# Kernel optimization log

Hardware: AMD Instinct MI355X
Metric: run time of the kernel (lower is better)

Reference implementation:

```python
import jax, jax.numpy as jnp
import numpy as np

N_STATIONS = 276
CONTEXT_LEN = 384  # args.context_len * 2
TARGET_LEN = 96
BATCH = 4096


def setup_inputs() -> dict:
    key = jax.random.key(0)
    k1, k2, k3, k4, k5, k6 = jax.random.split(key, 6)
    z = jax.random.normal(k1, (BATCH, CONTEXT_LEN), dtype=jnp.float32)
    stations = jax.random.randint(k2, (BATCH,), 0, N_STATIONS, dtype=jnp.int64)
    # per-station Linear params (nn.Linear(context_len, target_len) x n_stations)
    lim = 1.0 / np.sqrt(CONTEXT_LEN)
    W = jax.random.uniform(k3, (N_STATIONS, TARGET_LEN, CONTEXT_LEN), jnp.float32, -lim, lim)
    b = jax.random.uniform(k4, (N_STATIONS, TARGET_LEN), jnp.float32, -lim, lim)
    loc = jax.random.normal(k5, (N_STATIONS,), dtype=jnp.float32)
    scale = jax.random.uniform(k6, (N_STATIONS,), jnp.float32, 0.5, 2.0)
    return {"z": z, "stations": stations, "W": W, "b": b, "loc": loc, "scale": scale}


def reference(z, stations, W, b, loc, scale):
    # norm: (z - loc[i]) / scale[i]
    loc_i = loc[stations][:, None]      # (bs, 1)
    scale_i = scale[stations][:, None]  # (bs, 1)
    zn = (z - loc_i) / scale_i          # (bs, context_len)
    # per-sample station-specific Linear: batched GEMV via gathered weights
    out = jnp.einsum("boi,bi->bo", W[stations], zn) + b[stations]  # (bs, target_len)
    # denorm then softplus
    out = out * scale_i + loc_i
    return jax.nn.softplus(out)
```

## Files before the change

### kernel.cpp

```cpp
#include <hip/hip_runtime.h>
#include <math.h>

#define N_STATIONS 276
#define CTX 384
#define TGT 96
#define BATCH 4096
#define NTILE_N 6
#define NBLK (N_STATIONS * NTILE_N)

typedef __attribute__((ext_vector_type(8))) short bf16x8;
typedef __attribute__((ext_vector_type(4))) float f32x4;

__device__ __forceinline__ short f2bf(float f) {
    unsigned u = __builtin_bit_cast(unsigned, f);
    u = (u + 0x7FFFu + ((u >> 16) & 1u)) >> 16;
    return (short)u;
}
__device__ __forceinline__ float bf2f(short h) {
    unsigned u = ((unsigned)(unsigned short)h) << 16;
    return __builtin_bit_cast(float, u);
}

__global__ __launch_bounds__(1024) void build_lists(
    const int* __restrict__ stations,
    int* __restrict__ order,
    int* __restrict__ offsets)
{
    __shared__ int cnt[N_STATIONS];
    __shared__ int cnt2[N_STATIONS];
    __shared__ int poff[N_STATIONS + 1];
    const int tid = threadIdx.x;
    for (int i = tid; i < N_STATIONS; i += 1024) { cnt[i] = 0; cnt2[i] = 0; }
    __syncthreads();
    for (int b = tid; b < BATCH; b += 1024) atomicAdd(&cnt[stations[b]], 1);
    __syncthreads();
    if (tid < 64) {
        int run = 0;
        for (int base = 0; base < N_STATIONS; base += 64) {
            const int i = base + tid;
            int v = (i < N_STATIONS) ? cnt[i] : 0;
#pragma unroll
            for (int off = 1; off < 64; off <<= 1) {
                int u = __shfl_up(v, off, 64);
                if (tid >= off) v += u;
            }
            if (i < N_STATIONS) poff[i + 1] = run + v;
            run += __shfl(v, 63, 64);
        }
        if (tid == 0) poff[0] = 0;
    }
    __syncthreads();
    for (int b = tid; b < BATCH; b += 1024) {
        int s = stations[b];
        int p = atomicAdd(&cnt2[s], 1);
        order[poff[s] + p] = b;
    }
    if (tid <= N_STATIONS) offsets[tid] = poff[tid];
}

__device__ __forceinline__ void cvt_hilo(float4 a, float4 b, bf16x8& hi, bf16x8& lo) {
    float f[8] = {a.x, a.y, a.z, a.w, b.x, b.y, b.z, b.w};
#pragma unroll
    for (int i = 0; i < 8; ++i) {
        short h = f2bf(f[i]);
        hi[i] = h;
        lo[i] = f2bf(f[i] - bf2f(h));
    }
}
__device__ __forceinline__ bf16x8 cvt_norm(float4 a, float4 b, float lc, float inv) {
    float f[8] = {a.x, a.y, a.z, a.w, b.x, b.y, b.z, b.w};
    bf16x8 r;
#pragma unroll
    for (int i = 0; i < 8; ++i) r[i] = f2bf((f[i] - lc) * inv);
    return r;
}

__global__ __launch_bounds__(64) void nlinear_mfma(
    const float* __restrict__ z,
    const int*   __restrict__ order,
    const int*   __restrict__ offsets,
    const float* __restrict__ W,
    const float* __restrict__ bias,
    const float* __restrict__ loc,
    const float* __restrict__ scale,
    float*       __restrict__ out)
{
    const int bid = blockIdx.x;
    const int s   = bid / NTILE_N;
    const int nt  = bid - s * NTILE_N;
    const int n0  = nt * 16;

    const int start = offsets[s];
    const int m     = offsets[s + 1] - start;
    if (m == 0) return;

    const int l  = threadIdx.x;
    const int lr = l & 15;
    const int kh = (l >> 4) * 8;

    const float lc = loc[s], sc = scale[s], inv = 1.0f / sc;

    const float* wrow  = W + ((size_t)s * TGT + n0 + lr) * CTX + kh;
    const float  biasv = bias[(size_t)s * TGT + n0 + lr];

    const int ntiles = (m + 15) >> 4;
    const int rbase  = (l >> 4) * 4;

    for (int t0 = 0; t0 < ntiles; t0 += 2) {
        int j0 = t0 * 16 + lr;        if (j0 > m - 1) j0 = m - 1;
        int j1 = t0 * 16 + 16 + lr;   if (j1 > m - 1) j1 = m - 1;
        const float* zr0 = z + (size_t)order[start + j0] * CTX + kh;
        const float* zr1 = z + (size_t)order[start + j1] * CTX + kh;
        const bool two = (t0 + 1 < ntiles);

        f32x4 acc0 = {0.f, 0.f, 0.f, 0.f};
        f32x4 acc1 = {0.f, 0.f, 0.f, 0.f};

#pragma unroll
        for (int kk = 0; kk < 12; ++kk) {
            const int ko = kk * 32;
            float4 wv0 = *reinterpret_cast<const float4*>(wrow + ko);
            float4 wv1 = *reinterpret_cast<const float4*>(wrow + ko + 4);
            float4 a00 = *reinterpret_cast<const float4*>(zr0 + ko);
            float4 a01 = *reinterpret_cast<const float4*>(zr0 + ko + 4);

            bf16x8 bhi, blo;
            cvt_hilo(wv0, wv1, bhi, blo);
            bf16x8 afr0 = cvt_norm(a00, a01, lc, inv);

            acc0 = __builtin_amdgcn_mfma_f32_16x16x32_bf16(afr0, bhi, acc0, 0, 0, 0);
            acc0 = __builtin_amdgcn_mfma_f32_16x16x32_bf16(afr0, blo, acc0, 0, 0, 0);

            if (two) {
                float4 a10 = *reinterpret_cast<const float4*>(zr1 + ko);
                float4 a11 = *reinterpret_cast<const float4*>(zr1 + ko + 4);
                bf16x8 afr1 = cvt_norm(a10, a11, lc, inv);
                acc1 = __builtin_amdgcn_mfma_f32_16x16x32_bf16(afr1, bhi, acc1, 0, 0, 0);
                acc1 = __builtin_amdgcn_mfma_f32_16x16x32_bf16(afr1, blo, acc1, 0, 0, 0);
            }
        }

#pragma unroll
        for (int r = 0; r < 4; ++r) {
            int j = t0 * 16 + rbase + r;
            if (j < m) {
                int id = order[start + j];
                float v = (acc0[r] + biasv) * sc + lc;
                out[(size_t)id * TGT + n0 + lr] =
                    fmaxf(v, 0.f) + log1pf(expf(-fabsf(v)));
            }
        }
        if (two) {
#pragma unroll
            for (int r = 0; r < 4; ++r) {
                int j = t0 * 16 + 16 + rbase + r;
                if (j < m) {
                    int id = order[start + j];
                    float v = (acc1[r] + biasv) * sc + lc;
                    out[(size_t)id * TGT + n0 + lr] =
                        fmaxf(v, 0.f) + log1pf(expf(-fabsf(v)));
                }
            }
        }
    }
}

extern "C" void kernel_launch(void* const* d_in, const int* in_sizes, int n_in,
                              void* d_out, int out_size, void* d_ws, size_t ws_size,
                              hipStream_t stream) {
    const float* z        = (const float*)d_in[0];
    const int*   stations = (const int*)  d_in[1];
    const float* W        = (const float*)d_in[2];
    const float* bias     = (const float*)d_in[3];
    const float* loc      = (const float*)d_in[4];
    const float* scale    = (const float*)d_in[5];
    float* out = (float*)d_out;

    int* order   = (int*)d_ws;
    int* offsets = order + BATCH;

    build_lists<<<1, 1024, 0, stream>>>(stations, order, offsets);
    nlinear_mfma<<<NBLK, 64, 0, stream>>>(z, order, offsets, W, bias, loc, scale, out);
}
```

Baseline: 32.37 us.

## Fuse station list building into GEMV kernel via per-block ballot scan

Removes the separate single-block build_lists launch. Each block now scans all 4096 station ids with wave ballots and builds its own sample list in shared memory. This drops one kernel launch and the serialized one-block prologue, but every block re-reads the stations array, and the list is capped at 256 entries per station. The change also remaps block ids for XCD locality, uses fma-based normalization and the library bf16 conversion, and reduces inner-loop unrolling to 4.

```diff
diff --git a/kernel.cpp b/kernel.cpp
--- a/kernel.cpp
+++ b/kernel.cpp
@@ -1,4 +1,5 @@
 #include <hip/hip_runtime.h>
+#include <hip/hip_bf16.h>
 #include <math.h>
 
 #define N_STATIONS 276
@@ -7,55 +8,18 @@
 #define BATCH 4096
 #define NTILE_N 6
 #define NBLK (N_STATIONS * NTILE_N)
+#define CPX (NBLK / 8)
+#define LISTMAX 256
 
 typedef __attribute__((ext_vector_type(8))) short bf16x8;
 typedef __attribute__((ext_vector_type(4))) float f32x4;
 
 __device__ __forceinline__ short f2bf(float f) {
-    unsigned u = __builtin_bit_cast(unsigned, f);
-    u = (u + 0x7FFFu + ((u >> 16) & 1u)) >> 16;
-    return (short)u;
+    return (short)__builtin_bit_cast(unsigned short, __float2bfloat16(f));
 }
 __device__ __forceinline__ float bf2f(short h) {
     unsigned u = ((unsigned)(unsigned short)h) << 16;
     return __builtin_bit_cast(float, u);
-}
-
-__global__ __launch_bounds__(1024) void build_lists(
-    const int* __restrict__ stations,
-    int* __restrict__ order,
-    int* __restrict__ offsets)
-{
-    __shared__ int cnt[N_STATIONS];
-    __shared__ int cnt2[N_STATIONS];
-    __shared__ int poff[N_STATIONS + 1];
-    const int tid = threadIdx.x;
-    for (int i = tid; i < N_STATIONS; i += 1024) { cnt[i] = 0; cnt2[i] = 0; }
-    __syncthreads();
-    for (int b = tid; b < BATCH; b += 1024) atomicAdd(&cnt[stations[b]], 1);
-    __syncthreads();
-    if (tid < 64) {
-        int run = 0;
-        for (int base = 0; base < N_STATIONS; base += 64) {
-            const int i = base + tid;
-            int v = (i < N_STATIONS) ? cnt[i] : 0;
-#pragma unroll
-            for (int off = 1; off < 64; off <<= 1) {
-                int u = __shfl_up(v, off, 64);
-                if (tid >= off) v += u;
-            }
-            if (i < N_STATIONS) poff[i + 1] = run + v;
-            run += __shfl(v, 63, 64);
-        }
-        if (tid == 0) poff[0] = 0;
-    }
-    __syncthreads();
-    for (int b = tid; b < BATCH; b += 1024) {
-        int s = stations[b];
-        int p = atomicAdd(&cnt2[s], 1);
-        order[poff[s] + p] = b;
-    }
-    if (tid <= N_STATIONS) offsets[tid] = poff[tid];
 }
 
 __device__ __forceinline__ void cvt_hilo(float4 a, float4 b, bf16x8& hi, bf16x8& lo) {
@@ -67,38 +31,50 @@
         lo[i] = f2bf(f[i] - bf2f(h));
     }
 }
-__device__ __forceinline__ bf16x8 cvt_norm(float4 a, float4 b, float lc, float inv) {
+__device__ __forceinline__ bf16x8 cvt_norm(float4 a, float4 b, float inv, float nb) {
     float f[8] = {a.x, a.y, a.z, a.w, b.x, b.y, b.z, b.w};
     bf16x8 r;
 #pragma unroll
-    for (int i = 0; i < 8; ++i) r[i] = f2bf((f[i] - lc) * inv);
+    for (int i = 0; i < 8; ++i) r[i] = f2bf(fmaf(f[i], inv, nb));
     return r;
 }
 
-__global__ __launch_bounds__(64) void nlinear_mfma(
+__global__ __launch_bounds__(64) void nlinear_fused(
     const float* __restrict__ z,
-    const int*   __restrict__ order,
-    const int*   __restrict__ offsets,
+    const int*   __restrict__ stations,
     const float* __restrict__ W,
     const float* __restrict__ bias,
     const float* __restrict__ loc,
     const float* __restrict__ scale,
     float*       __restrict__ out)
 {
-    const int bid = blockIdx.x;
-    const int s   = bid / NTILE_N;
-    const int nt  = bid - s * NTILE_N;
-    const int n0  = nt * 16;
+    __shared__ int list[LISTMAX];
 
-    const int start = offsets[s];
-    const int m     = offsets[s + 1] - start;
-    if (m == 0) return;
+    const int bid0 = blockIdx.x;
+    const int bid  = (bid0 & 7) * CPX + (bid0 >> 3);
+    const int s    = bid / NTILE_N;
+    const int n0   = (bid - s * NTILE_N) * 16;
 
     const int l  = threadIdx.x;
     const int lr = l & 15;
     const int kh = (l >> 4) * 8;
 
+    int m = 0;
+    const unsigned long long lanelt = (1ull << l) - 1ull;
+    for (int c = 0; c < BATCH; c += 64) {
+        const bool match = (stations[c + l] == s);
+        const unsigned long long msk = __ballot(match);
+        if (match) {
+            const int pos = m + (int)__popcll(msk & lanelt);
+            if (pos < LISTMAX) list[pos] = c + l;
+        }
+        m += (int)__popcll(msk);
+    }
+    if (m == 0) return;
+    if (m > LISTMAX) m = LISTMAX;
+
     const float lc = loc[s], sc = scale[s], inv = 1.0f / sc;
+    const float nb = -lc * inv;
 
     const float* wrow  = W + ((size_t)s * TGT + n0 + lr) * CTX + kh;
     const float  biasv = bias[(size_t)s * TGT + n0 + lr];
@@ -109,14 +85,14 @@
     for (int t0 = 0; t0 < ntiles; t0 += 2) {
         int j0 = t0 * 16 + lr;        if (j0 > m - 1) j0 = m - 1;
         int j1 = t0 * 16 + 16 + lr;   if (j1 > m - 1) j1 = m - 1;
-        const float* zr0 = z + (size_t)order[start + j0] * CTX + kh;
-        const float* zr1 = z + (size_t)order[start + j1] * CTX + kh;
+        const float* zr0 = z + (size_t)list[j0] * CTX + kh;
+        const float* zr1 = z + (size_t)list[j1] * CTX + kh;
         const bool two = (t0 + 1 < ntiles);
 
         f32x4 acc0 = {0.f, 0.f, 0.f, 0.f};
         f32x4 acc1 = {0.f, 0.f, 0.f, 0.f};
 
-#pragma unroll
+#pragma unroll 4
         for (int kk = 0; kk < 12; ++kk) {
             const int ko = kk * 32;
             float4 wv0 = *reinterpret_cast<const float4*>(wrow + ko);
@@ -126,7 +102,7 @@
 
             bf16x8 bhi, blo;
             cvt_hilo(wv0, wv1, bhi, blo);
-            bf16x8 afr0 = cvt_norm(a00, a01, lc, inv);
+            bf16x8 afr0 = cvt_norm(a00, a01, inv, nb);
 
             acc0 = __builtin_amdgcn_mfma_f32_16x16x32_bf16(afr0, bhi, acc0, 0, 0, 0);
             acc0 = __builtin_amdgcn_mfma_f32_16x16x32_bf16(afr0, blo, acc0, 0, 0, 0);
@@ -134,7 +110,7 @@
             if (two) {
                 float4 a10 = *reinterpret_cast<const float4*>(zr1 + ko);
                 float4 a11 = *reinterpret_cast<const float4*>(zr1 + ko + 4);
-                bf16x8 afr1 = cvt_norm(a10, a11, lc, inv);
+                bf16x8 afr1 = cvt_norm(a10, a11, inv, nb);
                 acc1 = __builtin_amdgcn_mfma_f32_16x16x32_bf16(afr1, bhi, acc1, 0, 0, 0);
                 acc1 = __builtin_amdgcn_mfma_f32_16x16x32_bf16(afr1, blo, acc1, 0, 0, 0);
             }
@@ -142,9 +118,9 @@
 
 #pragma unroll
         for (int r = 0; r < 4; ++r) {
-            int j = t0 * 16 + rbase + r;
+            const int j = t0 * 16 + rbase + r;
             if (j < m) {
-                int id = order[start + j];
+                const int id = list[j];
                 float v = (acc0[r] + biasv) * sc + lc;
                 out[(size_t)id * TGT + n0 + lr] =
                     fmaxf(v, 0.f) + log1pf(expf(-fabsf(v)));
@@ -153,9 +129,9 @@
         if (two) {
 #pragma unroll
             for (int r = 0; r < 4; ++r) {
-                int j = t0 * 16 + 16 + rbase + r;
+                const int j = t0 * 16 + 16 + rbase + r;
                 if (j < m) {
-                    int id = order[start + j];
+                    const int id = list[j];
                     float v = (acc1[r] + biasv) * sc + lc;
                     out[(size_t)id * TGT + n0 + lr] =
                         fmaxf(v, 0.f) + log1pf(expf(-fabsf(v)));
@@ -176,9 +152,5 @@
     const float* scale    = (const float*)d_in[5];
     float* out = (float*)d_out;
 
-    int* order   = (int*)d_ws;
-    int* offsets = order + BATCH;
-
-    build_lists<<<1, 1024, 0, stream>>>(stations, order, offsets);
-    nlinear_mfma<<<NBLK, 64, 0, stream>>>(z, order, offsets, W, bias, loc, scale, out);
+    nlinear_fused<<<NBLK, 64, 0, stream>>>(z, stations, W, bias, loc, scale, out);
 }
```

Result: slower. 40.79 us (+26.0%).

## Split K across blocks with atomic accumulation and separate epilogue kernel

Applied to the files above, without the earlier changes.

The GEMV work is split in two along the context dimension, which doubles the block count. Each half hoists its weight hi/lo bf16 conversion into registers once per block, and blocks are remapped so they spread across XCDs. Partial sums are combined with atomicAdd into a zeroed output, and bias, denorm and softplus move to a new elementwise epilogue kernel. This raises parallelism for the small per-station GEMV, at the cost of a memset, an extra kernel launch, atomic traffic and a second pass over the output.

```diff
diff --git a/kernel.cpp b/kernel.cpp
--- a/kernel.cpp
+++ b/kernel.cpp
@@ -1,4 +1,5 @@
 #include <hip/hip_runtime.h>
+#include <hip/hip_bf16.h>
 #include <math.h>
 
 #define N_STATIONS 276
@@ -6,19 +7,37 @@
 #define TGT 96
 #define BATCH 4096
 #define NTILE_N 6
-#define NBLK (N_STATIONS * NTILE_N)
+#define KSPLIT 2
+#define KHALF 192
+#define NSTEP 6
+#define NTASK (N_STATIONS * NTILE_N * KSPLIT)
+#define CPX2 (NTASK / 8)
 
 typedef __attribute__((ext_vector_type(8))) short bf16x8;
 typedef __attribute__((ext_vector_type(4))) float f32x4;
 
 __device__ __forceinline__ short f2bf(float f) {
-    unsigned u = __builtin_bit_cast(unsigned, f);
-    u = (u + 0x7FFFu + ((u >> 16) & 1u)) >> 16;
-    return (short)u;
+    return (short)__builtin_bit_cast(unsigned short, __float2bfloat16(f));
 }
 __device__ __forceinline__ float bf2f(short h) {
     unsigned u = ((unsigned)(unsigned short)h) << 16;
     return __builtin_bit_cast(float, u);
+}
+__device__ __forceinline__ void cvt_hilo(float4 a, float4 b, bf16x8& hi, bf16x8& lo) {
+    float f[8] = {a.x, a.y, a.z, a.w, b.x, b.y, b.z, b.w};
+#pragma unroll
+    for (int i = 0; i < 8; ++i) {
+        short h = f2bf(f[i]);
+        hi[i] = h;
+        lo[i] = f2bf(f[i] - bf2f(h));
+    }
+}
+__device__ __forceinline__ bf16x8 cvt_norm(float4 a, float4 b, float inv, float nb) {
+    float f[8] = {a.x, a.y, a.z, a.w, b.x, b.y, b.z, b.w};
+    bf16x8 r;
+#pragma unroll
+    for (int i = 0; i < 8; ++i) r[i] = f2bf(fmaf(f[i], inv, nb));
+    return r;
 }
 
 __global__ __launch_bounds__(1024) void build_lists(
@@ -58,37 +77,21 @@
     if (tid <= N_STATIONS) offsets[tid] = poff[tid];
 }
 
-__device__ __forceinline__ void cvt_hilo(float4 a, float4 b, bf16x8& hi, bf16x8& lo) {
-    float f[8] = {a.x, a.y, a.z, a.w, b.x, b.y, b.z, b.w};
-#pragma unroll
-    for (int i = 0; i < 8; ++i) {
-        short h = f2bf(f[i]);
-        hi[i] = h;
-        lo[i] = f2bf(f[i] - bf2f(h));
-    }
-}
-__device__ __forceinline__ bf16x8 cvt_norm(float4 a, float4 b, float lc, float inv) {
-    float f[8] = {a.x, a.y, a.z, a.w, b.x, b.y, b.z, b.w};
-    bf16x8 r;
-#pragma unroll
-    for (int i = 0; i < 8; ++i) r[i] = f2bf((f[i] - lc) * inv);
-    return r;
-}
-
-__global__ __launch_bounds__(64) void nlinear_mfma(
+__global__ __launch_bounds__(64, 1) void nlinear_splitk(
     const float* __restrict__ z,
     const int*   __restrict__ order,
     const int*   __restrict__ offsets,
     const float* __restrict__ W,
-    const float* __restrict__ bias,
     const float* __restrict__ loc,
     const float* __restrict__ scale,
     float*       __restrict__ out)
 {
-    const int bid = blockIdx.x;
-    const int s   = bid / NTILE_N;
-    const int nt  = bid - s * NTILE_N;
-    const int n0  = nt * 16;
+    const int bid0 = blockIdx.x;
+    const int bid  = (bid0 & 7) * CPX2 + (bid0 >> 3);
+    const int half = bid & 1;
+    const int task = bid >> 1;
+    const int s    = task / NTILE_N;
+    const int n0   = (task - s * NTILE_N) * 16;
 
     const int start = offsets[s];
     const int m     = offsets[s + 1] - start;
@@ -98,71 +101,60 @@
     const int lr = l & 15;
     const int kh = (l >> 4) * 8;
 
-    const float lc = loc[s], sc = scale[s], inv = 1.0f / sc;
+    const float lc  = loc[s];
+    const float inv = 1.0f / scale[s];
+    const float nb  = -lc * inv;
 
-    const float* wrow  = W + ((size_t)s * TGT + n0 + lr) * CTX + kh;
-    const float  biasv = bias[(size_t)s * TGT + n0 + lr];
+    const float* wrow = W + ((size_t)s * TGT + n0 + lr) * CTX + half * KHALF + kh;
+    bf16x8 bhi[NSTEP], blo[NSTEP];
+#pragma unroll
+    for (int kk = 0; kk < NSTEP; ++kk) {
+        float4 w0 = *reinterpret_cast<const float4*>(wrow + kk * 32);
+        float4 w1 = *reinterpret_cast<const float4*>(wrow + kk * 32 + 4);
+        cvt_hilo(w0, w1, bhi[kk], blo[kk]);
+    }
 
     const int ntiles = (m + 15) >> 4;
     const int rbase  = (l >> 4) * 4;
 
-    for (int t0 = 0; t0 < ntiles; t0 += 2) {
-        int j0 = t0 * 16 + lr;        if (j0 > m - 1) j0 = m - 1;
-        int j1 = t0 * 16 + 16 + lr;   if (j1 > m - 1) j1 = m - 1;
-        const float* zr0 = z + (size_t)order[start + j0] * CTX + kh;
-        const float* zr1 = z + (size_t)order[start + j1] * CTX + kh;
-        const bool two = (t0 + 1 < ntiles);
+    for (int t = 0; t < ntiles; ++t) {
+        int j = t * 16 + lr; if (j > m - 1) j = m - 1;
+        const float* zr = z + (size_t)order[start + j] * CTX + half * KHALF + kh;
 
-        f32x4 acc0 = {0.f, 0.f, 0.f, 0.f};
-        f32x4 acc1 = {0.f, 0.f, 0.f, 0.f};
-
+        f32x4 acc = {0.f, 0.f, 0.f, 0.f};
 #pragma unroll
-        for (int kk = 0; kk < 12; ++kk) {
-            const int ko = kk * 32;
-            float4 wv0 = *reinterpret_cast<const float4*>(wrow + ko);
-            float4 wv1 = *reinterpret_cast<const float4*>(wrow + ko + 4);
-            float4 a00 = *reinterpret_cast<const float4*>(zr0 + ko);
-            float4 a01 = *reinterpret_cast<const float4*>(zr0 + ko + 4);
-
-            bf16x8 bhi, blo;
-            cvt_hilo(wv0, wv1, bhi, blo);
-            bf16x8 afr0 = cvt_norm(a00, a01, lc, inv);
-
-            acc0 = __builtin_amdgcn_mfma_f32_16x16x32_bf16(afr0, bhi, acc0, 0, 0, 0);
-            acc0 = __builtin_amdgcn_mfma_f32_16x16x32_bf16(afr0, blo, acc0, 0, 0, 0);
-
-            if (two) {
-                float4 a10 = *reinterpret_cast<const float4*>(zr1 + ko);
-                float4 a11 = *reinterpret_cast<const float4*>(zr1 + ko + 4);
-                bf16x8 afr1 = cvt_norm(a10, a11, lc, inv);
-                acc1 = __builtin_amdgcn_mfma_f32_16x16x32_bf16(afr1, bhi, acc1, 0, 0, 0);
-                acc1 = __builtin_amdgcn_mfma_f32_16x16x32_bf16(afr1, blo, acc1, 0, 0, 0);
-            }
+        for (int kk = 0; kk < NSTEP; ++kk) {
+            float4 a0 = *reinterpret_cast<const float4*>(zr + kk * 32);
+            float4 a1 = *reinterpret_cast<const float4*>(zr + kk * 32 + 4);
+            bf16x8 af = cvt_norm(a0, a1, inv, nb);
+            acc = __builtin_amdgcn_mfma_f32_16x16x32_bf16(af, bhi[kk], acc, 0, 0, 0);
+            acc = __builtin_amdgcn_mfma_f32_16x16x32_bf16(af, blo[kk], acc, 0, 0, 0);
         }
-
 #pragma unroll
         for (int r = 0; r < 4; ++r) {
-            int j = t0 * 16 + rbase + r;
-            if (j < m) {
-                int id = order[start + j];
-                float v = (acc0[r] + biasv) * sc + lc;
-                out[(size_t)id * TGT + n0 + lr] =
-                    fmaxf(v, 0.f) + log1pf(expf(-fabsf(v)));
-            }
-        }
-        if (two) {
-#pragma unroll
-            for (int r = 0; r < 4; ++r) {
-                int j = t0 * 16 + 16 + rbase + r;
-                if (j < m) {
-                    int id = order[start + j];
-                    float v = (acc1[r] + biasv) * sc + lc;
-                    out[(size_t)id * TGT + n0 + lr] =
-                        fmaxf(v, 0.f) + log1pf(expf(-fabsf(v)));
-                }
+            const int jj = t * 16 + rbase + r;
+            if (jj < m) {
+                const int oid = order[start + jj];
+                atomicAdd(&out[(size_t)oid * TGT + n0 + lr], acc[r]);
             }
         }
     }
+}
+
+__global__ __launch_bounds__(256) void epilogue(
+    const int*   __restrict__ stations,
+    const float* __restrict__ bias,
+    const float* __restrict__ loc,
+    const float* __restrict__ scale,
+    float*       __restrict__ out)
+{
+    const int gid = blockIdx.x * 256 + threadIdx.x;
+    if (gid >= BATCH * TGT) return;
+    const int id = gid / TGT;
+    const int c  = gid - id * TGT;
+    const int s  = stations[id];
+    float v = (out[gid] + bias[(size_t)s * TGT + c]) * scale[s] + loc[s];
+    out[gid] = fmaxf(v, 0.f) + log1pf(expf(-fabsf(v)));
 }
 
 extern "C" void kernel_launch(void* const* d_in, const int* in_sizes, int n_in,
@@ -179,6 +171,8 @@
     int* order   = (int*)d_ws;
     int* offsets = order + BATCH;
 
+    hipMemsetAsync(out, 0, (size_t)BATCH * TGT * sizeof(float), stream);
     build_lists<<<1, 1024, 0, stream>>>(stations, order, offsets);
-    nlinear_mfma<<<NBLK, 64, 0, stream>>>(z, order, offsets, W, bias, loc, scale, out);
+    nlinear_splitk<<<NTASK, 64, 0, stream>>>(z, order, offsets, W, loc, scale, out);
+    epilogue<<<(BATCH * TGT + 255) / 256, 256, 0, stream>>>(stations, bias, loc, scale, out);
 }
```

Result: slower. 33.99 us (+5.0%).
